# Kernel tuning notes

Measured on AMD Instinct MI355X. Metric: run time of the kernel, lower is better.

Reference implementation:

```python
import jax, jax.numpy as jnp
import numpy as np
from jax import lax

B, T, N, H, NC = 2, 8, 512, 64, 10
NEG = -1e9
LN_EPS = 1e-5


def _gatv2(x, mask, Wl, Wr, att, b):
    # GATv2Conv (PyG semantics, eval mode): e_ij = att . leaky_relu(Wr x_i + Wl x_j),
    # softmax over source nodes j with self-loops, out_i = sum_j alpha_ij * (Wl x_j).
    # x: (B, N, Fin); mask: (N, N) bool adjacency incl. self-loops; att: (heads, C).
    heads, C = att.shape
    Bn, Nn, _ = x.shape
    xl = (x @ Wl).reshape(Bn, Nn, heads, C)  # source transform
    xr = (x @ Wr).reshape(Bn, Nn, heads, C)  # target transform
    s = jax.nn.leaky_relu(xr[:, :, None] + xl[:, None, :], 0.2)  # (B, Ni, Nj, h, C)
    e = jnp.einsum('bijhc,hc->bijh', s, att)
    e = jnp.where(mask[None, :, :, None], e, NEG)
    alpha = jax.nn.softmax(e, axis=2)  # softmax over neighbors j
    out = jnp.einsum('bijh,bjhc->bihc', alpha, xl)
    return out.reshape(Bn, Nn, heads * C) + b


def _gru_layer(x, Wih, Whh, bih, bhh):
    # torch nn.GRU single layer, batch_first; x: (B, T, Hin)
    h0 = jnp.zeros((x.shape[0], Whh.shape[0]), x.dtype)
    def step(h, xt):
        gi = xt @ Wih + bih
        gh = h @ Whh + bhh
        ir, iz, inn = jnp.split(gi, 3, axis=-1)
        hr, hz, hn = jnp.split(gh, 3, axis=-1)
        r = jax.nn.sigmoid(ir + hr)
        z = jax.nn.sigmoid(iz + hz)
        n = jnp.tanh(inn + r * hn)
        hnew = (1.0 - z) * n + z * h
        return hnew, hnew
    _, ys = lax.scan(step, h0, jnp.swapaxes(x, 0, 1))
    return jnp.swapaxes(ys, 0, 1)


def setup_inputs() -> dict:
    key = jax.random.key(0)
    ks = jax.random.split(key, 20)
    def rn(i, shape, s=0.1):
        return jax.random.normal(ks[i], shape, jnp.float32) * s
    x_seq = jax.random.normal(ks[0], (B, T, N, 1), jnp.float32)
    a = jax.random.uniform(ks[1], (N, N))
    up = jnp.triu((a > 0.95).astype(jnp.float32), 1)
    static_adj = up + up.T  # sparse symmetric 0/1 static graph
    dyn_W = jax.random.normal(ks[2], (N, N), jnp.float32)
    reg_lambda = jnp.array([0.05], jnp.float32)
    return {
        'x_seq': x_seq, 'static_adj': static_adj, 'dyn_W': dyn_W, 'reg_lambda': reg_lambda,
        'g1_Wl': rn(3, (1, H)), 'g1_Wr': rn(4, (1, H)), 'g1_att': rn(5, (4, H // 4)), 'g1_b': jnp.zeros(H),
        'g2_Wl': rn(6, (H, H)), 'g2_Wr': rn(7, (H, H)), 'g2_att': rn(8, (1, H)), 'g2_b': jnp.zeros(H),
        'gru_Wih0': rn(9, (H, 3 * H)), 'gru_Whh0': rn(10, (H, 3 * H)), 'gru_bih0': jnp.zeros(3 * H), 'gru_bhh0': jnp.zeros(3 * H),
        'gru_Wih1': rn(11, (H, 3 * H)), 'gru_Whh1': rn(12, (H, 3 * H)), 'gru_bih1': jnp.zeros(3 * H), 'gru_bhh1': jnp.zeros(3 * H),
        'attn_W': rn(13, (H, 1)), 'attn_b': jnp.zeros(1),
        'cls_W1': rn(14, (H, H)), 'cls_b1': jnp.zeros(H), 'ln_g': jnp.ones(H), 'ln_b': jnp.zeros(H),
        'cls_W2': rn(15, (H, NC)), 'cls_b2': jnp.zeros(NC),
    }


def reference(x_seq, static_adj, dyn_W, reg_lambda,
              g1_Wl, g1_Wr, g1_att, g1_b, g2_Wl, g2_Wr, g2_att, g2_b,
              gru_Wih0, gru_Whh0, gru_bih0, gru_bhh0,
              gru_Wih1, gru_Whh1, gru_bih1, gru_bhh1,
              attn_W, attn_b, cls_W1, cls_b1, ln_g, ln_b, cls_W2, cls_b2):
    Bn, Tn, Nn, _ = x_seq.shape
    lam = jnp.maximum(reg_lambda[0], 0.01)
    t = jnp.arange(Tn, dtype=x_seq.dtype)
    gts = jnp.exp(-lam * t)  # gating values per timestep
    dyn = jax.nn.relu(dyn_W + dyn_W.T)
    fused = gts[:, None, None] * static_adj + (1.0 - gts)[:, None, None] * dyn  # (T, N, N)
    masks = (fused > 0) | jnp.eye(Nn, dtype=bool)[None]  # edge set + self-loops

    def step(carry, inp):
        xt, mask = inp  # xt: (B, N, 1)
        h = jax.nn.elu(_gatv2(xt, mask, g1_Wl, g1_Wr, g1_att, g1_b))
        h = jax.nn.elu(_gatv2(h, mask, g2_Wl, g2_Wr, g2_att, g2_b))
        return carry, h.mean(axis=1)  # (B, H) graph readout

    _, reps = lax.scan(step, 0.0, (jnp.swapaxes(x_seq, 0, 1), masks))
    h_seq = jnp.swapaxes(reps, 0, 1)  # (B, T, H)

    gru_out = _gru_layer(h_seq, gru_Wih0, gru_Whh0, gru_bih0, gru_bhh0)
    gru_out = _gru_layer(gru_out, gru_Wih1, gru_Whh1, gru_bih1, gru_bhh1)

    att_scores = jax.nn.softmax((gru_out @ attn_W + attn_b)[..., 0], axis=1)  # (B, T)
    final = jnp.einsum('bt,bth->bh', att_scores, gru_out)

    z = final @ cls_W1 + cls_b1
    mu = jnp.mean(z, axis=-1, keepdims=True)
    var = jnp.var(z, axis=-1, keepdims=True)
    z = (z - mu) / jnp.sqrt(var + LN_EPS) * ln_g + ln_b
    z = jax.nn.gelu(z, approximate=False)
    logits = z @ cls_W2 + cls_b2
    return logits, gts, att_scores
```

## Files before the change

### kernel.cpp

```cpp
#include <hip/hip_runtime.h>
#include <math.h>

#define BB 2
#define TT 8
#define NN 512
#define HH 64
#define NC 10

typedef unsigned char uchar;

__device__ __forceinline__ float elu1(float v){ return v > 0.f ? v : expm1f(v); }
__device__ __forceinline__ float sigm(float v){ return 1.f/(1.f+expf(-v)); }

__global__ __launch_bounds__(256) void k_mask(
    const float* __restrict__ dW, const float* __restrict__ sadj,
    uchar* __restrict__ M0, uchar* __restrict__ M1,
    float* __restrict__ Z2, float* __restrict__ hseq,
    const float* __restrict__ att1, const float* __restrict__ Wr1,
    const float* __restrict__ Wl1, float* __restrict__ AB,
    const float* __restrict__ Whh0, const float* __restrict__ Wih1,
    const float* __restrict__ Whh1, float4* __restrict__ WT4)
{
    __shared__ float tr[64][65];
    int bx = blockIdx.x, by = blockIdx.y;
    int tid = threadIdx.x;
    if (blockIdx.z == 1){
        int idx = (by*8 + bx)*256 + tid;
        if (idx < 3*4096){
            int m = idx >> 12, r = idx & 4095;
            int gg = r >> 6, k = r & 63;
            const float* W = (m == 0) ? Whh0 : (m == 1) ? Wih1 : Whh1;
            float4 o;
            o.x = W[k*192 + gg];
            o.y = W[k*192 + 64 + gg];
            o.z = W[k*192 + 128 + gg];
            o.w = 0.f;
            WT4[(size_t)m*4096 + r] = o;
        }
        return;
    }
    int i0 = by*64, j0 = bx*64;
    #pragma unroll
    for (int q = 0; q < 4; ++q){
        int r = (tid >> 4) + 16*q, c4 = tid & 15;
        float4 v = *(const float4*)&dW[(size_t)(j0+r)*NN + i0 + 4*c4];
        tr[r][4*c4+0] = v.x; tr[r][4*c4+1] = v.y;
        tr[r][4*c4+2] = v.z; tr[r][4*c4+3] = v.w;
    }
    __syncthreads();
    #pragma unroll
    for (int q = 0; q < 4; ++q){
        int row = (tid >> 4) + 16*q, c4 = tid & 15;
        int i = i0 + row, j = j0 + 4*c4;
        float4 d  = *(const float4*)&dW[(size_t)i*NN + j];
        float4 sa = *(const float4*)&sadj[(size_t)i*NN + j];
        uchar4 m0, m1;
        float dd0 = d.x + tr[4*c4+0][row];
        float dd1 = d.y + tr[4*c4+1][row];
        float dd2 = d.z + tr[4*c4+2][row];
        float dd3 = d.w + tr[4*c4+3][row];
        m0.x = (sa.x > 0.f) || (i == j+0);
        m0.y = (sa.y > 0.f) || (i == j+1);
        m0.z = (sa.z > 0.f) || (i == j+2);
        m0.w = (sa.w > 0.f) || (i == j+3);
        m1.x = m0.x || (dd0 > 0.f);
        m1.y = m0.y || (dd1 > 0.f);
        m1.z = m0.z || (dd2 > 0.f);
        m1.w = m0.w || (dd3 > 0.f);
        *(uchar4*)&M0[(size_t)i*NN + j] = m0;
        *(uchar4*)&M1[(size_t)i*NN + j] = m1;
    }
    int flat = (by*8 + bx)*256 + tid;
    if (flat < BB*TT*NN) Z2[flat] = 0.f;
    else if (flat < BB*TT*NN + BB*TT*HH) hseq[flat - BB*TT*NN] = 0.f;
    if (bx == 0 && by == 0 && tid < 8){
        int h = tid & 3;
        const float* W = (tid < 4) ? Wr1 : Wl1;
        float s = 0.f;
        for (int c = 0; c < 16; ++c) s += att1[h*16+c]*W[h*16+c];
        AB[tid] = s;
    }
}

__global__ __launch_bounds__(256) void k_gat1f(
    const float* __restrict__ x_seq, const uchar* __restrict__ M0,
    const uchar* __restrict__ M1,
    const float* __restrict__ Wl, const float* __restrict__ Wr,
    const float* __restrict__ att, const float* __restrict__ bias,
    const float* __restrict__ AB,
    const float* __restrict__ Wl2, const float* __restrict__ Wr2,
    const float* __restrict__ att2,
    float* __restrict__ xl2, float* __restrict__ xr2,
    float* __restrict__ ui, float* __restrict__ vj)
{
    __shared__ float x_s[NN];
    __shared__ float S_s[4][4];
    __shared__ float h_s[4][HH];
    __shared__ float Wl2_s[64*64];
    __shared__ float Wr2_s[64*64];
    int bt = blockIdx.y; int t = bt % TT;
    int i0 = blockIdx.x * 4;
    int tid = threadIdx.x;
    int il = tid >> 6, jl = tid & 63;
    int i = i0 + il;
    const uchar* M = t ? M1 : M0;
    ((float2*)x_s)[tid] = ((const float2*)(x_seq + bt*NN))[tid];
    #pragma unroll
    for (int q = 0; q < 4; ++q){
        int idx = q*256 + tid;
        ((float4*)Wl2_s)[idx] = ((const float4*)Wl2)[idx];
        ((float4*)Wr2_s)[idx] = ((const float4*)Wr2)[idx];
    }
    __syncthreads();
    float xi = x_s[i];
    const uchar* Mrow = M + (size_t)i*NN;
    float xj[8], msk[8];
    #pragma unroll
    for (int jj = 0; jj < 8; ++jj){
        int j = jj*64 + jl;
        xj[jj] = x_s[j];
        msk[jj] = Mrow[j] ? 1.f : 0.f;
    }
    float sw[4] = {0,0,0,0}, swx[4] = {0,0,0,0};
    for (int h = 0; h < 4; ++h){
        float acc[8] = {0,0,0,0,0,0,0,0};
        #pragma unroll
        for (int c = 0; c < 16; ++c){
            int hc = h*16 + c;
            float wl = Wl[hc];
            float q  = 0.4f * att[hc];
            float pr = xi * Wr[hc];
            #pragma unroll
            for (int jj = 0; jj < 8; ++jj){
                float s = fmaf(xj[jj], wl, pr);
                acc[jj] = fmaf(q, fabsf(s), acc[jj]);
            }
        }
        float lin = 0.6f * xi * AB[h];
        float al6 = 0.6f * AB[4+h];
        #pragma unroll
        for (int jj = 0; jj < 8; ++jj){
            float e = acc[jj] + fmaf(al6, xj[jj], lin);
            float w = msk[jj] * __expf(e);
            sw[h] += w;
            swx[h] = fmaf(w, xj[jj], swx[h]);
        }
    }
    #pragma unroll
    for (int off = 32; off; off >>= 1){
        #pragma unroll
        for (int h = 0; h < 4; ++h){
            sw[h]  += __shfl_down(sw[h],  off);
            swx[h] += __shfl_down(swx[h], off);
        }
    }
    if (jl == 0){
        #pragma unroll
        for (int h = 0; h < 4; ++h) S_s[il][h] = swx[h] / sw[h];
    }
    __syncthreads();
    {
        int hc = tid & 63, row = tid >> 6;
        float v = S_s[row][hc >> 4] * Wl[hc] + bias[hc];
        h_s[row][hc] = elu1(v);
    }
    __syncthreads();
    {
        int c = tid & 63, row = tid >> 6;
        float al = 0.f, ar = 0.f;
        #pragma unroll 8
        for (int k = 0; k < 64; ++k){
            float hv = h_s[row][k];
            al = fmaf(hv, Wl2_s[k*64 + c], al);
            ar = fmaf(hv, Wr2_s[k*64 + c], ar);
        }
        size_t ridx = (size_t)(bt*NN + i0 + row);
        xl2[ridx*HH + c] = al;
        xr2[ridx*HH + c] = ar;
        float a2 = att2[c];
        float pu = a2 * ar, pv = a2 * al;
        #pragma unroll
        for (int off = 32; off; off >>= 1){
            pu += __shfl_down(pu, off);
            pv += __shfl_down(pv, off);
        }
        if (c == 0){ ui[ridx] = pu; vj[ridx] = pv; }
    }
}

__global__ __launch_bounds__(256) void k_e2(
    const float* __restrict__ xl2, const float* __restrict__ xr2,
    const uchar* __restrict__ M0, const uchar* __restrict__ M1,
    const float* __restrict__ att,
    const float* __restrict__ ui, const float* __restrict__ vj,
    float* __restrict__ WgT, float* __restrict__ Z2)
{
    __shared__ float xrT[64][68];
    __shared__ float xlT[64][68];
    int bt = blockIdx.z, t = bt % TT;
    int i0 = blockIdx.y*64, j0 = blockIdx.x*64;
    int base = bt*NN;
    int tid = threadIdx.x;
    const uchar* M = t ? M1 : M0;
    {
        int r = tid >> 2;
        #pragma unroll
        for (int q = 0; q < 4; ++q){
            int c4 = (tid & 3) + 4*q;
            float4 a = *(const float4*)&xr2[(size_t)(base+i0+r)*HH + 4*c4];
            float4 b = *(const float4*)&xl2[(size_t)(base+j0+r)*HH + 4*c4];
            xrT[4*c4+0][r] = a.x; xrT[4*c4+1][r] = a.y;
            xrT[4*c4+2][r] = a.z; xrT[4*c4+3][r] = a.w;
            xlT[4*c4+0][r] = b.x; xlT[4*c4+1][r] = b.y;
            xlT[4*c4+2][r] = b.z; xlT[4*c4+3][r] = b.w;
        }
    }
    int ti = tid >> 4, tj = tid & 15;
    int iL = ti*4, jL = tj*4;
    float4 u4 = *(const float4*)&ui[base+i0+iL];
    float4 v4 = *(const float4*)&vj[base+j0+jL];
    float uu[4] = {u4.x, u4.y, u4.z, u4.w};
    float vv[4] = {v4.x, v4.y, v4.z, v4.w};
    float acc[4][4];
    #pragma unroll
    for (int ii = 0; ii < 4; ++ii)
        #pragma unroll
        for (int jj = 0; jj < 4; ++jj)
            acc[ii][jj] = 0.6f*(uu[ii] + vv[jj]);
    __syncthreads();
    #pragma unroll 8
    for (int c = 0; c < 64; ++c){
        float qa = 0.4f * att[c];
        float4 a4 = *(const float4*)&xrT[c][iL];
        float4 b4 = *(const float4*)&xlT[c][jL];
        float a[4] = {a4.x, a4.y, a4.z, a4.w};
        float b[4] = {b4.x, b4.y, b4.z, b4.w};
        #pragma unroll
        for (int ii = 0; ii < 4; ++ii)
            #pragma unroll
            for (int jj = 0; jj < 4; ++jj)
                acc[ii][jj] = fmaf(qa, fabsf(a[ii] + b[jj]), acc[ii][jj]);
    }
    float w[4][4];
    #pragma unroll
    for (int ii = 0; ii < 4; ++ii){
        int i = i0 + iL + ii;
        uchar4 mr = *(const uchar4*)&M[(size_t)i*NN + j0 + jL];
        w[ii][0] = mr.x ? __expf(acc[ii][0]) : 0.f;
        w[ii][1] = mr.y ? __expf(acc[ii][1]) : 0.f;
        w[ii][2] = mr.z ? __expf(acc[ii][2]) : 0.f;
        w[ii][3] = mr.w ? __expf(acc[ii][3]) : 0.f;
    }
    #pragma unroll
    for (int jj = 0; jj < 4; ++jj){
        int j = j0 + jL + jj;
        float4 wv = { w[0][jj], w[1][jj], w[2][jj], w[3][jj] };
        *(float4*)&WgT[(size_t)(base+j)*NN + i0 + iL] = wv;
    }
    #pragma unroll
    for (int ii = 0; ii < 4; ++ii){
        float zi = w[ii][0] + w[ii][1] + w[ii][2] + w[ii][3];
        zi += __shfl_down(zi, 8);
        zi += __shfl_down(zi, 4);
        zi += __shfl_down(zi, 2);
        zi += __shfl_down(zi, 1);
        if (tj == 0) atomicAdd(&Z2[base + i0 + iL + ii], zi);
    }
}

__global__ __launch_bounds__(256) void k_a2(
    const float* __restrict__ WgT, const float* __restrict__ xl2,
    const float* __restrict__ Z2, const float* __restrict__ bias,
    float* __restrict__ hseq)
{
    __shared__ float a_s[64][20];
    __shared__ float x_s[64][68];
    __shared__ float msum[64];
    int bt = blockIdx.y;
    int i0 = blockIdx.x * 16;
    int base = bt * NN;
    int tid = threadIdx.x;
    int tg = tid >> 4, tc = tid & 15;
    if (tid < 64) msum[tid] = 0.f;
    float4 acc = {0,0,0,0};
    for (int jc = 0; jc < 8; ++jc){
        int j0 = jc*64;
        {
            int row = tid >> 2, c4 = tid & 3;
            ((float4*)&a_s[row][0])[c4] = ((const float4*)&WgT[(size_t)(base+j0+row)*NN + i0])[c4];
        }
        #pragma unroll
        for (int q = 0; q < 4; ++q){
            int idx = q*256 + tid; int row = idx >> 4, c4 = idx & 15;
            ((float4*)&x_s[row][0])[c4] = ((const float4*)&xl2[(size_t)(base+j0+row)*HH])[c4];
        }
        __syncthreads();
        #pragma unroll 8
        for (int j = 0; j < 64; ++j){
            float a = a_s[j][tg];
            float4 xv = ((float4*)&x_s[j][0])[tc];
            acc.x = fmaf(a, xv.x, acc.x);
            acc.y = fmaf(a, xv.y, acc.y);
            acc.z = fmaf(a, xv.z, acc.z);
            acc.w = fmaf(a, xv.w, acc.w);
        }
        __syncthreads();
    }
    float rz = 1.f / Z2[base + i0 + tg];
    float4 b4 = ((const float4*)bias)[tc];
    float4 h;
    h.x = elu1(acc.x*rz + b4.x);
    h.y = elu1(acc.y*rz + b4.y);
    h.z = elu1(acc.z*rz + b4.z);
    h.w = elu1(acc.w*rz + b4.w);
    atomicAdd(&msum[tc*4+0], h.x);
    atomicAdd(&msum[tc*4+1], h.y);
    atomicAdd(&msum[tc*4+2], h.z);
    atomicAdd(&msum[tc*4+3], h.w);
    __syncthreads();
    if (tid < 64) atomicAdd(&hseq[bt*HH + tid], msum[tid]*(1.f/(float)NN));
}

__global__ __launch_bounds__(256) void k_pre(
    const float* __restrict__ hseq, const float* __restrict__ Wih0,
    const float* __restrict__ bih0, float* __restrict__ gi0)
{
    int idx = blockIdx.x*256 + threadIdx.x;
    int bt = idx / 192, g = idx % 192;
    const float* x = hseq + bt*HH;
    float acc = bih0[g];
    #pragma unroll 8
    for (int k = 0; k < HH; ++k)
        acc = fmaf(x[k], Wih0[k*192 + g], acc);
    gi0[idx] = acc;
}

#define P4 65
__global__ __launch_bounds__(512) void k_gru2(
    const float* __restrict__ gi0, const float4* __restrict__ WT4,
    const float* __restrict__ bhh0,
    const float* __restrict__ bih1, const float* __restrict__ bhh1,
    const float* __restrict__ lamp, const float* __restrict__ attn_W,
    const float* __restrict__ attn_b, const float* __restrict__ W1,
    const float* __restrict__ b1, const float* __restrict__ ln_g,
    const float* __restrict__ ln_b, const float* __restrict__ W2,
    const float* __restrict__ b2, float* __restrict__ out)
{
    __shared__ float4 WA[64*P4];
    __shared__ float4 WB[64*P4];
    __shared__ float gi_s[BB*TT*192];
    __shared__ float y_s[BB*TT*HH];
    __shared__ float sc_s[BB][TT], at_s[BB][TT];
    __shared__ float fin_s[BB][HH], z_s[BB][HH], g_s[BB][HH];
    __shared__ float mu_s[BB], iv_s[BB];
    int tid = threadIdx.x;
    int wave = tid >> 6, lane = tid & 63;
    for (int v = tid; v < 4096; v += 512){
        WA[(v >> 6)*P4 + (v & 63)] = WT4[v];
        WB[(v >> 6)*P4 + (v & 63)] = WT4[4096 + v];
    }
    for (int v = tid; v < BB*TT*192; v += 512) gi_s[v] = gi0[v];
    __syncthreads();
    float y[TT];
    float g1r[TT], g1z[TT], g1n[TT];
    if (wave < 2){
        int b = wave;
        float bhr = bhh0[lane], bhz = bhh0[64+lane], bhn = bhh0[128+lane];
        float h = 0.f;
        for (int t = 0; t < TT; ++t){
            float ghr = bhr, ghz = bhz, ghn = bhn;
            #pragma unroll 16
            for (int k = 0; k < 64; ++k){
                float4 w4 = WA[lane*P4 + k];
                float hk = __shfl(h, k);
                ghr = fmaf(w4.x, hk, ghr);
                ghz = fmaf(w4.y, hk, ghz);
                ghn = fmaf(w4.z, hk, ghn);
            }
            const float* gi = &gi_s[(b*TT + t)*192];
            float r = sigm(gi[lane] + ghr);
            float z = sigm(gi[64+lane] + ghz);
            float n = tanhf(gi[128+lane] + r*ghn);
            h = (1.f - z)*n + z*h;
            y[t] = h;
        }
        float bi1r = bih1[lane], bi1z = bih1[64+lane], bi1n = bih1[128+lane];
        #pragma unroll
        for (int t = 0; t < TT; ++t){ g1r[t] = bi1r; g1z[t] = bi1z; g1n[t] = bi1n; }
        #pragma unroll 8
        for (int k = 0; k < 64; ++k){
            float4 w4 = WB[lane*P4 + k];
            #pragma unroll
            for (int t = 0; t < TT; ++t){
                float yk = __shfl(y[t], k);
                g1r[t] = fmaf(w4.x, yk, g1r[t]);
                g1z[t] = fmaf(w4.y, yk, g1z[t]);
                g1n[t] = fmaf(w4.z, yk, g1n[t]);
            }
        }
    }
    __syncthreads();
    if (wave >= 2){
        for (int v = tid - 128; v < 4096; v += 384)
            WA[(v >> 6)*P4 + (v & 63)] = WT4[2*4096 + v];
    }
    __syncthreads();
    if (wave < 2){
        int b = wave;
        float bhr = bhh1[lane], bhz = bhh1[64+lane], bhn = bhh1[128+lane];
        float h = 0.f;
        for (int t = 0; t < TT; ++t){
            float ghr = bhr, ghz = bhz, ghn = bhn;
            #pragma unroll 16
            for (int k = 0; k < 64; ++k){
                float4 w4 = WA[lane*P4 + k];
                float hk = __shfl(h, k);
                ghr = fmaf(w4.x, hk, ghr);
                ghz = fmaf(w4.y, hk, ghz);
                ghn = fmaf(w4.z, hk, ghn);
            }
            float r = sigm(g1r[t] + ghr);
            float z = sigm(g1z[t] + ghz);
            float n = tanhf(g1n[t] + r*ghn);
            h = (1.f - z)*n + z*h;
            y_s[(b*TT + t)*HH + lane] = h;
        }
    }
    __syncthreads();
    float lam = fmaxf(lamp[0], 0.01f);
    if (tid < TT) out[BB*NC + tid] = expf(-lam*(float)tid);
    if (tid < BB*TT){
        int bb = tid >> 3, t = tid & 7;
        float s = attn_b[0];
        const float* r = &y_s[(bb*TT+t)*HH];
        for (int h = 0; h < HH; ++h) s += r[h]*attn_W[h];
        sc_s[bb][t] = s;
    }
    __syncthreads();
    if (tid < BB){
        float mx = -INFINITY;
        for (int t = 0; t < TT; ++t) mx = fmaxf(mx, sc_s[tid][t]);
        float se = 0.f;
        for (int t = 0; t < TT; ++t){ float w = expf(sc_s[tid][t]-mx); at_s[tid][t] = w; se += w; }
        for (int t = 0; t < TT; ++t){
            at_s[tid][t] /= se;
            out[BB*NC + TT + tid*TT + t] = at_s[tid][t];
        }
    }
    __syncthreads();
    if (tid < BB*HH){
        int bb = tid >> 6, h = tid & 63;
        float a = 0.f;
        for (int t = 0; t < TT; ++t) a += at_s[bb][t]*y_s[(bb*TT+t)*HH + h];
        fin_s[bb][h] = a;
    }
    __syncthreads();
    if (tid < BB*HH){
        int bb = tid >> 6, h = tid & 63;
        float a = b1[h];
        for (int k = 0; k < HH; ++k) a += fin_s[bb][k]*W1[k*HH+h];
        z_s[bb][h] = a;
    }
    __syncthreads();
    if (tid < BB){
        float mu = 0.f;
        for (int h = 0; h < HH; ++h) mu += z_s[tid][h];
        mu *= (1.f/HH);
        float v = 0.f;
        for (int h = 0; h < HH; ++h){ float d = z_s[tid][h]-mu; v += d*d; }
        v *= (1.f/HH);
        mu_s[tid] = mu; iv_s[tid] = 1.f/sqrtf(v + 1e-5f);
    }
    __syncthreads();
    if (tid < BB*HH){
        int bb = tid >> 6, h = tid & 63;
        float zn = (z_s[bb][h]-mu_s[bb])*iv_s[bb]*ln_g[h] + ln_b[h];
        g_s[bb][h] = 0.5f*zn*(1.f + erff(zn*0.70710678118654752f));
    }
    __syncthreads();
    if (tid < BB*NC){
        int bb = tid / NC, c = tid % NC;
        float a = b2[c];
        for (int k = 0; k < HH; ++k) a += g_s[bb][k]*W2[k*NC+c];
        out[bb*NC + c] = a;
    }
}

extern "C" void kernel_launch(void* const* d_in, const int* in_sizes, int n_in,
                              void* d_out, int out_size, void* d_ws, size_t ws_size,
                              hipStream_t stream)
{
    const float* x_seq = (const float*)d_in[0];
    const float* sadj  = (const float*)d_in[1];
    const float* dynW  = (const float*)d_in[2];
    const float* lamp  = (const float*)d_in[3];
    const float* g1_Wl = (const float*)d_in[4];
    const float* g1_Wr = (const float*)d_in[5];
    const float* g1_att= (const float*)d_in[6];
    const float* g1_b  = (const float*)d_in[7];
    const float* g2_Wl = (const float*)d_in[8];
    const float* g2_Wr = (const float*)d_in[9];
    const float* g2_att= (const float*)d_in[10];
    const float* g2_b  = (const float*)d_in[11];
    const float* Wih0  = (const float*)d_in[12];
    const float* Whh0  = (const float*)d_in[13];
    const float* bih0  = (const float*)d_in[14];
    const float* bhh0  = (const float*)d_in[15];
    const float* Wih1  = (const float*)d_in[16];
    const float* Whh1  = (const float*)d_in[17];
    const float* bih1  = (const float*)d_in[18];
    const float* bhh1  = (const float*)d_in[19];
    const float* attnW = (const float*)d_in[20];
    const float* attnb = (const float*)d_in[21];
    const float* W1    = (const float*)d_in[22];
    const float* b1    = (const float*)d_in[23];
    const float* lng   = (const float*)d_in[24];
    const float* lnb   = (const float*)d_in[25];
    const float* W2    = (const float*)d_in[26];
    const float* b2    = (const float*)d_in[27];
    float* out = (float*)d_out;

    const int RWS = BB*TT*NN*HH;
    uchar* M0 = (uchar*)d_ws;
    uchar* M1 = M0 + (size_t)NN*NN;
    float* fb = (float*)(M1 + (size_t)NN*NN);
    float* Z2   = fb;
    float* AB   = Z2   + BB*TT*NN;
    float* ui   = AB   + 16;
    float* vj   = ui   + BB*TT*NN;
    float* xl2  = vj   + BB*TT*NN;
    float* xr2  = xl2  + RWS;
    float* WgT  = xr2  + RWS;
    float* hseq = WgT  + (size_t)BB*TT*NN*NN;
    float* gi0  = hseq + BB*TT*HH;
    float4* WT4 = (float4*)(gi0 + BB*TT*192);

    k_mask <<<dim3(8,8,2), 256, 0, stream>>>(dynW, sadj, M0, M1, Z2, hseq, g1_att, g1_Wr, g1_Wl, AB,
                                             Whh0, Wih1, Whh1, WT4);
    k_gat1f<<<dim3(NN/4, BB*TT), 256, 0, stream>>>(x_seq, M0, M1, g1_Wl, g1_Wr, g1_att, g1_b, AB,
                                                   g2_Wl, g2_Wr, g2_att, xl2, xr2, ui, vj);
    k_e2   <<<dim3(NN/64, NN/64, BB*TT), 256, 0, stream>>>(xl2, xr2, M0, M1, g2_att, ui, vj, WgT, Z2);
    k_a2   <<<dim3(NN/16, BB*TT), 256, 0, stream>>>(WgT, xl2, Z2, g2_b, hseq);
    k_pre  <<<12, 256, 0, stream>>>(hseq, Wih0, bih0, gi0);
    k_gru2 <<<1, 512, 0, stream>>>(gi0, WT4, bhh0, bih1, bhh1,
                                   lamp, attnW, attnb, W1, b1, lng, lnb, W2, b2, out);
}
```

Before: 228.5 us.

## Fuse GAT layer-2 score, softmax and aggregation into one kernel

```diff
diff --git a/kernel.cpp b/kernel.cpp
--- a/kernel.cpp
+++ b/kernel.cpp
@@ -15,7 +15,7 @@
 __global__ __launch_bounds__(256) void k_mask(
     const float* __restrict__ dW, const float* __restrict__ sadj,
     uchar* __restrict__ M0, uchar* __restrict__ M1,
-    float* __restrict__ Z2, float* __restrict__ hseq,
+    float* __restrict__ hseq,
     const float* __restrict__ att1, const float* __restrict__ Wr1,
     const float* __restrict__ Wl1, float* __restrict__ AB,
     const float* __restrict__ Whh0, const float* __restrict__ Wih1,
@@ -71,8 +71,7 @@
         *(uchar4*)&M1[(size_t)i*NN + j] = m1;
     }
     int flat = (by*8 + bx)*256 + tid;
-    if (flat < BB*TT*NN) Z2[flat] = 0.f;
-    else if (flat < BB*TT*NN + BB*TT*HH) hseq[flat - BB*TT*NN] = 0.f;
+    if (flat < BB*TT*HH) hseq[flat] = 0.f;
     if (bx == 0 && by == 0 && tid < 8){
         int h = tid & 3;
         const float* W = (tid < 4) ? Wr1 : Wl1;
@@ -188,156 +187,179 @@
     }
 }
 
-__global__ __launch_bounds__(256) void k_e2(
+__global__ __launch_bounds__(256) void k_gat2(
     const float* __restrict__ xl2, const float* __restrict__ xr2,
     const uchar* __restrict__ M0, const uchar* __restrict__ M1,
-    const float* __restrict__ att,
-    const float* __restrict__ ui, const float* __restrict__ vj,
-    float* __restrict__ WgT, float* __restrict__ Z2)
+    const float* __restrict__ att, const float* __restrict__ ui,
+    const float* __restrict__ vj, const float* __restrict__ bias,
+    float* __restrict__ hseq)
 {
-    __shared__ float xrT[64][68];
-    __shared__ float xlT[64][68];
-    int bt = blockIdx.z, t = bt % TT;
-    int i0 = blockIdx.y*64, j0 = blockIdx.x*64;
-    int base = bt*NN;
+    __shared__ float xl_s[128][68];
+    __shared__ float wT_s[128][36];
+    __shared__ float xrT_s[64][36];
+    __shared__ float v_s[128];
+    __shared__ float u_s[32];
+    __shared__ float z_s[32];
+    __shared__ float q_s[64];
+
+    int bt = blockIdx.y, t = bt & 7;
+    int i0 = blockIdx.x * 32;
+    int base = bt * NN;
     int tid = threadIdx.x;
     const uchar* M = t ? M1 : M0;
-    {
-        int r = tid >> 2;
-        #pragma unroll
-        for (int q = 0; q < 4; ++q){
-            int c4 = (tid & 3) + 4*q;
-            float4 a = *(const float4*)&xr2[(size_t)(base+i0+r)*HH + 4*c4];
-            float4 b = *(const float4*)&xl2[(size_t)(base+j0+r)*HH + 4*c4];
-            xrT[4*c4+0][r] = a.x; xrT[4*c4+1][r] = a.y;
-            xrT[4*c4+2][r] = a.z; xrT[4*c4+3][r] = a.w;
-            xlT[4*c4+0][r] = b.x; xlT[4*c4+1][r] = b.y;
-            xlT[4*c4+2][r] = b.z; xlT[4*c4+3][r] = b.w;
-        }
-    }
-    int ti = tid >> 4, tj = tid & 15;
-    int iL = ti*4, jL = tj*4;
-    float4 u4 = *(const float4*)&ui[base+i0+iL];
-    float4 v4 = *(const float4*)&vj[base+j0+jL];
-    float uu[4] = {u4.x, u4.y, u4.z, u4.w};
-    float vv[4] = {v4.x, v4.y, v4.z, v4.w};
-    float acc[4][4];
-    #pragma unroll
-    for (int ii = 0; ii < 4; ++ii)
-        #pragma unroll
-        for (int jj = 0; jj < 4; ++jj)
-            acc[ii][jj] = 0.6f*(uu[ii] + vv[jj]);
-    __syncthreads();
-    #pragma unroll 8
-    for (int c = 0; c < 64; ++c){
-        float qa = 0.4f * att[c];
-        float4 a4 = *(const float4*)&xrT[c][iL];
-        float4 b4 = *(const float4*)&xlT[c][jL];
-        float a[4] = {a4.x, a4.y, a4.z, a4.w};
-        float b[4] = {b4.x, b4.y, b4.z, b4.w};
-        #pragma unroll
-        for (int ii = 0; ii < 4; ++ii)
+
+    #pragma unroll
+    for (int q = 0; q < 2; ++q){
+        int idx = q*256 + tid;
+        int row = idx >> 4, c4 = idx & 15;
+        float4 xv = ((const float4*)&xr2[(size_t)(base+i0+row)*HH])[c4];
+        xrT_s[c4*4+0][row] = xv.x;
+        xrT_s[c4*4+1][row] = xv.y;
+        xrT_s[c4*4+2][row] = xv.z;
+        xrT_s[c4*4+3][row] = xv.w;
+    }
+    if (tid < 32) u_s[tid] = ui[base + i0 + tid];
+    if (tid < 64) q_s[tid] = 0.4f * att[tid];
+
+    int ig = tid >> 5, jg = tid & 31;
+    int wv = tid >> 6, ln = tid & 63;
+    int ig2 = ln >> 3, cg2 = ln & 7;
+
+    float zreg[4] = {0.f,0.f,0.f,0.f};
+    float acc[4][8];
+    #pragma unroll
+    for (int a = 0; a < 4; ++a)
+        #pragma unroll
+        for (int r = 0; r < 8; ++r) acc[a][r] = 0.f;
+
+    for (int tile = 0; tile < 4; ++tile){
+        int j0 = tile * 128;
+        __syncthreads();
+        #pragma unroll
+        for (int q = 0; q < 8; ++q){
+            int idx = q*256 + tid;
+            int row = idx >> 4, c4 = idx & 15;
+            ((float4*)&xl_s[row][0])[c4] = ((const float4*)&xl2[(size_t)(base+j0+row)*HH])[c4];
+        }
+        if (tid < 128) v_s[tid] = vj[base + j0 + tid];
+        __syncthreads();
+        float e[4][4];
+        {
+            float u0 = 0.6f*u_s[ig*4+0], u1 = 0.6f*u_s[ig*4+1];
+            float u2 = 0.6f*u_s[ig*4+2], u3 = 0.6f*u_s[ig*4+3];
+            #pragma unroll
+            for (int jj = 0; jj < 4; ++jj){
+                float vv = 0.6f * v_s[jj*32 + jg];
+                e[0][jj] = u0 + vv; e[1][jj] = u1 + vv;
+                e[2][jj] = u2 + vv; e[3][jj] = u3 + vv;
+            }
+        }
+        #pragma unroll 4
+        for (int c4 = 0; c4 < 16; ++c4){
+            float q4[4], xr4[4][4], xl4[4][4];
+            *(float4*)q4 = *(const float4*)&q_s[c4*4];
+            #pragma unroll
+            for (int k = 0; k < 4; ++k)
+                *(float4*)xr4[k] = *(const float4*)&xrT_s[c4*4+k][ig*4];
             #pragma unroll
             for (int jj = 0; jj < 4; ++jj)
-                acc[ii][jj] = fmaf(qa, fabsf(a[ii] + b[jj]), acc[ii][jj]);
-    }
-    float w[4][4];
-    #pragma unroll
-    for (int ii = 0; ii < 4; ++ii){
-        int i = i0 + iL + ii;
-        uchar4 mr = *(const uchar4*)&M[(size_t)i*NN + j0 + jL];
-        w[ii][0] = mr.x ? __expf(acc[ii][0]) : 0.f;
-        w[ii][1] = mr.y ? __expf(acc[ii][1]) : 0.f;
-        w[ii][2] = mr.z ? __expf(acc[ii][2]) : 0.f;
-        w[ii][3] = mr.w ? __expf(acc[ii][3]) : 0.f;
-    }
-    #pragma unroll
-    for (int jj = 0; jj < 4; ++jj){
-        int j = j0 + jL + jj;
-        float4 wv = { w[0][jj], w[1][jj], w[2][jj], w[3][jj] };
-        *(float4*)&WgT[(size_t)(base+j)*NN + i0 + iL] = wv;
-    }
-    #pragma unroll
-    for (int ii = 0; ii < 4; ++ii){
-        float zi = w[ii][0] + w[ii][1] + w[ii][2] + w[ii][3];
-        zi += __shfl_down(zi, 8);
-        zi += __shfl_down(zi, 4);
-        zi += __shfl_down(zi, 2);
-        zi += __shfl_down(zi, 1);
-        if (tj == 0) atomicAdd(&Z2[base + i0 + iL + ii], zi);
-    }
-}
-
-__global__ __launch_bounds__(256) void k_a2(
-    const float* __restrict__ WgT, const float* __restrict__ xl2,
-    const float* __restrict__ Z2, const float* __restrict__ bias,
-    float* __restrict__ hseq)
-{
-    __shared__ float a_s[64][20];
-    __shared__ float x_s[64][68];
-    __shared__ float msum[64];
-    int bt = blockIdx.y;
-    int i0 = blockIdx.x * 16;
-    int base = bt * NN;
-    int tid = threadIdx.x;
-    int tg = tid >> 4, tc = tid & 15;
-    if (tid < 64) msum[tid] = 0.f;
-    float4 acc = {0,0,0,0};
-    for (int jc = 0; jc < 8; ++jc){
-        int j0 = jc*64;
-        {
-            int row = tid >> 2, c4 = tid & 3;
-            ((float4*)&a_s[row][0])[c4] = ((const float4*)&WgT[(size_t)(base+j0+row)*NN + i0])[c4];
-        }
-        #pragma unroll
-        for (int q = 0; q < 4; ++q){
-            int idx = q*256 + tid; int row = idx >> 4, c4 = idx & 15;
-            ((float4*)&x_s[row][0])[c4] = ((const float4*)&xl2[(size_t)(base+j0+row)*HH])[c4];
+                *(float4*)xl4[jj] = ((const float4*)&xl_s[jj*32+jg][0])[c4];
+            #pragma unroll
+            for (int jj = 0; jj < 4; ++jj)
+                #pragma unroll
+                for (int k = 0; k < 4; ++k){
+                    float xc = xl4[jj][k];
+                    #pragma unroll
+                    for (int ii = 0; ii < 4; ++ii)
+                        e[ii][jj] = fmaf(q4[k], fabsf(xr4[k][ii] + xc), e[ii][jj]);
+                }
+        }
+        #pragma unroll
+        for (int jj = 0; jj < 4; ++jj){
+            int j = jj*32 + jg;
+            float w0, w1, w2, w3;
+            {
+                uchar m0 = M[(size_t)(i0 + ig*4 + 0)*NN + j0 + j];
+                uchar m1 = M[(size_t)(i0 + ig*4 + 1)*NN + j0 + j];
+                uchar m2 = M[(size_t)(i0 + ig*4 + 2)*NN + j0 + j];
+                uchar m3 = M[(size_t)(i0 + ig*4 + 3)*NN + j0 + j];
+                w0 = m0 ? __expf(e[0][jj]) : 0.f;
+                w1 = m1 ? __expf(e[1][jj]) : 0.f;
+                w2 = m2 ? __expf(e[2][jj]) : 0.f;
+                w3 = m3 ? __expf(e[3][jj]) : 0.f;
+            }
+            zreg[0] += w0; zreg[1] += w1; zreg[2] += w2; zreg[3] += w3;
+            float4 wq; wq.x = w0; wq.y = w1; wq.z = w2; wq.w = w3;
+            *(float4*)&wT_s[j][ig*4] = wq;
         }
         __syncthreads();
-        #pragma unroll 8
-        for (int j = 0; j < 64; ++j){
-            float a = a_s[j][tg];
-            float4 xv = ((float4*)&x_s[j][0])[tc];
-            acc.x = fmaf(a, xv.x, acc.x);
-            acc.y = fmaf(a, xv.y, acc.y);
-            acc.z = fmaf(a, xv.z, acc.z);
-            acc.w = fmaf(a, xv.w, acc.w);
-        }
-        __syncthreads();
-    }
-    float rz = 1.f / Z2[base + i0 + tg];
-    float4 b4 = ((const float4*)bias)[tc];
-    float4 h;
-    h.x = elu1(acc.x*rz + b4.x);
-    h.y = elu1(acc.y*rz + b4.y);
-    h.z = elu1(acc.z*rz + b4.z);
-    h.w = elu1(acc.w*rz + b4.w);
-    atomicAdd(&msum[tc*4+0], h.x);
-    atomicAdd(&msum[tc*4+1], h.y);
-    atomicAdd(&msum[tc*4+2], h.z);
-    atomicAdd(&msum[tc*4+3], h.w);
-    __syncthreads();
-    if (tid < 64) atomicAdd(&hseq[bt*HH + tid], msum[tid]*(1.f/(float)NN));
-}
-
-__global__ __launch_bounds__(256) void k_pre(
-    const float* __restrict__ hseq, const float* __restrict__ Wih0,
-    const float* __restrict__ bih0, float* __restrict__ gi0)
-{
-    int idx = blockIdx.x*256 + threadIdx.x;
-    int bt = idx / 192, g = idx % 192;
-    const float* x = hseq + bt*HH;
-    float acc = bih0[g];
-    #pragma unroll 8
-    for (int k = 0; k < HH; ++k)
-        acc = fmaf(x[k], Wih0[k*192 + g], acc);
-    gi0[idx] = acc;
+        #pragma unroll 4
+        for (int jj = 0; jj < 32; ++jj){
+            int j = wv*32 + jj;
+            float w4[4], xa[8];
+            *(float4*)w4      = *(const float4*)&wT_s[j][ig2*4];
+            *(float4*)&xa[0]  = ((const float4*)&xl_s[j][0])[cg2*2+0];
+            *(float4*)&xa[4]  = ((const float4*)&xl_s[j][0])[cg2*2+1];
+            #pragma unroll
+            for (int a = 0; a < 4; ++a)
+                #pragma unroll
+                for (int r = 0; r < 8; ++r)
+                    acc[a][r] = fmaf(w4[a], xa[r], acc[a][r]);
+        }
+    }
+    __syncthreads();
+    #pragma unroll
+    for (int off = 16; off; off >>= 1){
+        #pragma unroll
+        for (int ii = 0; ii < 4; ++ii) zreg[ii] += __shfl_down(zreg[ii], off, 32);
+    }
+    if (jg == 0){
+        #pragma unroll
+        for (int ii = 0; ii < 4; ++ii) z_s[ig*4+ii] = zreg[ii];
+    }
+    float* scratch = &xl_s[0][0];
+    if (wv > 0){
+        #pragma unroll
+        for (int a = 0; a < 4; ++a)
+            #pragma unroll
+            for (int r = 0; r < 8; ++r)
+                scratch[(a*8+r)*192 + (wv-1)*64 + ln] = acc[a][r];
+    }
+    __syncthreads();
+    if (wv == 0){
+        float pm[8];
+        #pragma unroll
+        for (int r = 0; r < 8; ++r) pm[r] = 0.f;
+        #pragma unroll
+        for (int a = 0; a < 4; ++a){
+            float rz = 1.f / z_s[ig2*4 + a];
+            #pragma unroll
+            for (int r = 0; r < 8; ++r){
+                float s = acc[a][r]
+                        + scratch[(a*8+r)*192 +   0 + ln]
+                        + scratch[(a*8+r)*192 +  64 + ln]
+                        + scratch[(a*8+r)*192 + 128 + ln];
+                float h = elu1(s*rz + bias[cg2*8 + r]);
+                pm[r] += h;
+            }
+        }
+        #pragma unroll
+        for (int off = 32; off >= 8; off >>= 1){
+            #pragma unroll
+            for (int r = 0; r < 8; ++r) pm[r] += __shfl_down(pm[r], off);
+        }
+        if (ig2 == 0){
+            #pragma unroll
+            for (int r = 0; r < 8; ++r)
+                atomicAdd(&hseq[bt*HH + cg2*8 + r], pm[r] * (1.f/(float)NN));
+        }
+    }
 }
 
 #define P4 65
 __global__ __launch_bounds__(512) void k_gru2(
-    const float* __restrict__ gi0, const float4* __restrict__ WT4,
+    const float* __restrict__ hseq, const float* __restrict__ Wih0,
+    const float* __restrict__ bih0, const float4* __restrict__ WT4,
     const float* __restrict__ bhh0,
     const float* __restrict__ bih1, const float* __restrict__ bhh1,
     const float* __restrict__ lamp, const float* __restrict__ attn_W,
@@ -349,6 +371,7 @@
     __shared__ float4 WA[64*P4];
     __shared__ float4 WB[64*P4];
     __shared__ float gi_s[BB*TT*192];
+    __shared__ float hs_s[BB*TT*HH];
     __shared__ float y_s[BB*TT*HH];
     __shared__ float sc_s[BB][TT], at_s[BB][TT];
     __shared__ float fin_s[BB][HH], z_s[BB][HH], g_s[BB][HH];
@@ -359,7 +382,18 @@
         WA[(v >> 6)*P4 + (v & 63)] = WT4[v];
         WB[(v >> 6)*P4 + (v & 63)] = WT4[4096 + v];
     }
-    for (int v = tid; v < BB*TT*192; v += 512) gi_s[v] = gi0[v];
+    for (int v = tid; v < BB*TT*HH; v += 512) hs_s[v] = hseq[v];
+    __syncthreads();
+    #pragma unroll
+    for (int o = 0; o < 6; ++o){
+        int idx = o*512 + tid;
+        int b = idx / 192, g = idx % 192;
+        float a = bih0[g];
+        const float* hr = &hs_s[b*HH];
+        #pragma unroll 8
+        for (int k = 0; k < HH; ++k) a = fmaf(hr[k], Wih0[k*192 + g], a);
+        gi_s[idx] = a;
+    }
     __syncthreads();
     float y[TT];
     float g1r[TT], g1z[TT], g1n[TT];
@@ -524,24 +558,19 @@
     uchar* M0 = (uchar*)d_ws;
     uchar* M1 = M0 + (size_t)NN*NN;
     float* fb = (float*)(M1 + (size_t)NN*NN);
-    float* Z2   = fb;
-    float* AB   = Z2   + BB*TT*NN;
+    float* AB   = fb;
     float* ui   = AB   + 16;
     float* vj   = ui   + BB*TT*NN;
     float* xl2  = vj   + BB*TT*NN;
     float* xr2  = xl2  + RWS;
-    float* WgT  = xr2  + RWS;
-    float* hseq = WgT  + (size_t)BB*TT*NN*NN;
-    float* gi0  = hseq + BB*TT*HH;
-    float4* WT4 = (float4*)(gi0 + BB*TT*192);
-
-    k_mask <<<dim3(8,8,2), 256, 0, stream>>>(dynW, sadj, M0, M1, Z2, hseq, g1_att, g1_Wr, g1_Wl, AB,
+    float* hseq = xr2  + RWS;
+    float4* WT4 = (float4*)(hseq + BB*TT*HH);
+
+    k_mask <<<dim3(8,8,2), 256, 0, stream>>>(dynW, sadj, M0, M1, hseq, g1_att, g1_Wr, g1_Wl, AB,
                                              Whh0, Wih1, Whh1, WT4);
     k_gat1f<<<dim3(NN/4, BB*TT), 256, 0, stream>>>(x_seq, M0, M1, g1_Wl, g1_Wr, g1_att, g1_b, AB,
                                                    g2_Wl, g2_Wr, g2_att, xl2, xr2, ui, vj);
-    k_e2   <<<dim3(NN/64, NN/64, BB*TT), 256, 0, stream>>>(xl2, xr2, M0, M1, g2_att, ui, vj, WgT, Z2);
-    k_a2   <<<dim3(NN/16, BB*TT), 256, 0, stream>>>(WgT, xl2, Z2, g2_b, hseq);
-    k_pre  <<<12, 256, 0, stream>>>(hseq, Wih0, bih0, gi0);
-    k_gru2 <<<1, 512, 0, stream>>>(gi0, WT4, bhh0, bih1, bhh1,
+    k_gat2 <<<dim3(NN/32, BB*TT), 256, 0, stream>>>(xl2, xr2, M0, M1, g2_att, ui, vj, g2_b, hseq);
+    k_gru2 <<<1, 512, 0, stream>>>(hseq, Wih0, bih0, WT4, bhh0, bih1, bhh1,
                                    lamp, attnW, attnb, W1, b1, lng, lnb, W2, b2, out);
 }
```

Measured after the change: 229.5 us. About the same (+0.4%).
